# Optimization experiments

Measured on AMD Instinct MI355X. Metric: run time of the kernel, lower is better.

The kernel has to match this reference:

```python
import jax, jax.numpy as jnp
import numpy as np

B, TI, TO = 32, 128, 64
VI, VO = 32000, 32000
E, H, A = 256, 512, 512
EOS, BOS = 0, 1


def setup_inputs() -> dict:
    key = jax.random.key(0)
    ks = jax.random.split(key, 24)
    def p(k, shape):
        return jax.random.normal(k, shape, jnp.float32) * 0.05
    return {
        "inp": jax.random.randint(ks[0], (B, TI), 0, VI),
        "out": jax.random.randint(ks[1], (B, TO), 0, VO),
        "emb_inp": p(ks[2], (VI, E)),
        "emb_out": p(ks[3], (VO, E)),
        "enc_Wih_f": p(ks[4], (3 * H, E)),
        "enc_Whh_f": p(ks[5], (3 * H, H)),
        "enc_bih_f": p(ks[6], (3 * H,)),
        "enc_bhh_f": p(ks[7], (3 * H,)),
        "enc_Wih_b": p(ks[8], (3 * H, E)),
        "enc_Whh_b": p(ks[9], (3 * H, H)),
        "enc_bih_b": p(ks[10], (3 * H,)),
        "enc_bhh_b": p(ks[11], (3 * H,)),
        "dec_start_W": p(ks[12], (H, 2 * H)),
        "dec_start_b": p(ks[13], (H,)),
        "dec_Wih": p(ks[14], (3 * H, E + 2 * H)),
        "dec_Whh": p(ks[15], (3 * H, H)),
        "dec_bih": p(ks[16], (3 * H,)),
        "dec_bhh": p(ks[17], (3 * H,)),
        "attn_Wenc": p(ks[18], (A, 2 * H)),
        "attn_benc": p(ks[19], (A,)),
        "attn_Wdec": p(ks[20], (A, H)),
        "attn_bdec": p(ks[21], (A,)),
        "attn_v": p(ks[22], (A,)),
        "attn_vb": jnp.zeros((), jnp.float32),
        "logits_W": p(ks[23], (VO, 3 * H)),
        "logits_b": jnp.zeros((VO,), jnp.float32),
    }


def _gru_dir(x, Wih, bih, Whh, bhh, reverse):
    # x: [B,T,E]; precompute input projections once: [B,T,3H]
    xp = jnp.einsum('bte,ge->btg', x, Wih) + bih
    Hd = Whh.shape[1]
    def step(h, xt):
        gh = h @ Whh.T + bhh
        xr, xz, xn = jnp.split(xt, 3, -1)
        hr, hz, hn = jnp.split(gh, 3, -1)
        r = jax.nn.sigmoid(xr + hr)
        z = jax.nn.sigmoid(xz + hz)
        n = jnp.tanh(xn + r * hn)
        h_new = (1.0 - z) * n + z * h
        return h_new, h_new
    h0 = jnp.zeros((x.shape[0], Hd), x.dtype)
    _, hs = jax.lax.scan(step, h0, jnp.swapaxes(xp, 0, 1), reverse=reverse)
    return jnp.swapaxes(hs, 0, 1)  # [B,T,H]


def _forward(inp, out, emb_inp, emb_out,
             enc_Wih_f, enc_Whh_f, enc_bih_f, enc_bhh_f,
             enc_Wih_b, enc_Whh_b, enc_bih_b, enc_bhh_b,
             dec_start_W, dec_start_b, dec_Wih, dec_Whh, dec_bih, dec_bhh,
             attn_Wenc, attn_benc, attn_Wdec, attn_bdec, attn_v, attn_vb,
             logits_W, logits_b):
    x = emb_inp[inp]  # [B,TI,E]
    ef = _gru_dir(x, enc_Wih_f, enc_bih_f, enc_Whh_f, enc_bhh_f, False)
    eb = _gru_dir(x, enc_Wih_b, enc_bih_b, enc_Whh_b, enc_bhh_b, True)
    enc = jnp.concatenate([ef, eb], -1)  # [B,TI,2H]
    mask = (inp != EOS).astype(jnp.float32)
    lengths = jnp.minimum(mask.sum(1).astype(jnp.int32), TI - 1)
    last = enc[jnp.arange(enc.shape[0]), lengths]  # [B,2H]
    dec0 = last @ dec_start_W.T + dec_start_b  # [B,H]
    enc_proj = jnp.einsum('btd,ad->bta', enc, attn_Wenc) + attn_benc  # [B,TI,A]

    def attend(dec):
        dp = dec @ attn_Wdec.T + attn_bdec  # [B,A]
        s = jnp.tanh(enc_proj + dp[:, None, :]) @ attn_v + attn_vb  # [B,TI]
        s = jnp.where(mask > 0, s, -jnp.inf)
        pr = jax.nn.softmax(s, -1)
        return jnp.einsum('bt,btd->bd', pr, enc), pr

    a0, _ = attend(dec0)

    def step(carry, tok):
        h, a = carry
        e = emb_out[tok]  # [B,E]
        xg = jnp.concatenate([e, a], -1) @ dec_Wih.T + dec_bih
        hg = h @ dec_Whh.T + dec_bhh
        xr, xz, xn = jnp.split(xg, 3, -1)
        hr, hz, hn = jnp.split(hg, 3, -1)
        r = jax.nn.sigmoid(xr + hr)
        z = jax.nn.sigmoid(xz + hz)
        n = jnp.tanh(xn + r * hn)
        h_new = (1.0 - z) * n + z * h
        a_new, _ = attend(h_new)
        lg = jnp.concatenate([h_new, a_new], -1) @ logits_W.T + logits_b
        return (h_new, a_new), lg

    toks = jnp.swapaxes(out[:, :-1], 0, 1)  # [TO-1, B]
    _, lgs = jax.lax.scan(step, (dec0, a0), toks)  # [TO-1,B,VO]
    first = jnp.log(jax.nn.one_hot(jnp.full((out.shape[0],), BOS), VO) + 1e-9)
    return jnp.swapaxes(jnp.concatenate([first[None], lgs], 0), 0, 1)  # [B,TO,VO]


def reference(inp, out, emb_inp, emb_out,
              enc_Wih_f, enc_Whh_f, enc_bih_f, enc_bhh_f,
              enc_Wih_b, enc_Whh_b, enc_bih_b, enc_bhh_b,
              dec_start_W, dec_start_b, dec_Wih, dec_Whh, dec_bih, dec_bhh,
              attn_Wenc, attn_benc, attn_Wdec, attn_bdec, attn_v, attn_vb,
              logits_W, logits_b):
    return _forward(inp, out, emb_inp, emb_out,
                    enc_Wih_f, enc_Whh_f, enc_bih_f, enc_bhh_f,
                    enc_Wih_b, enc_Whh_b, enc_bih_b, enc_bhh_b,
                    dec_start_W, dec_start_b, dec_Wih, dec_Whh, dec_bih, dec_bhh,
                    attn_Wenc, attn_benc, attn_Wdec, attn_bdec, attn_v, attn_vb,
                    logits_W, logits_b)
```

## Files before the change

kernel.cpp:

```cpp
#include <hip/hip_runtime.h>
#include <math.h>
#include <stdint.h>

#define B_   32
#define TI_  128
#define TO_  64
#define E_   256
#define H_   512
#define A_   512
#define VO_  32000
#define G3_  1536
#define D2H_ 1024

using short8 = __attribute__((ext_vector_type(8))) short;
using f32x4  = __attribute__((ext_vector_type(4))) float;

__device__ __forceinline__ unsigned short f2bf(float x) {
  uint32_t u = __builtin_bit_cast(uint32_t, x);
  uint32_t r = (u + 0x7fffu + ((u >> 16) & 1u)) >> 16;
  return (unsigned short)r;
}


__global__ __launch_bounds__(256) void k_zero(float* __restrict__ p, int n) {
  int i = blockIdx.x * 256 + threadIdx.x;
  if (i < n) p[i] = 0.f;
}

__global__ __launch_bounds__(256) void k_zero_u16(unsigned short* __restrict__ p, int n) {
  int i = blockIdx.x * 256 + threadIdx.x;
  if (i < n) p[i] = 0;
}

__global__ __launch_bounds__(256) void k_cvt_bf16(const float* __restrict__ in,
                                                  unsigned short* __restrict__ out, int n8) {
  int i = blockIdx.x * 256 + threadIdx.x;
  if (i >= n8) return;
  float4 a = ((const float4*)in)[2 * i];
  float4 b = ((const float4*)in)[2 * i + 1];
  ushort4 lo = make_ushort4(f2bf(a.x), f2bf(a.y), f2bf(a.z), f2bf(a.w));
  ushort4 hi = make_ushort4(f2bf(b.x), f2bf(b.y), f2bf(b.z), f2bf(b.w));
  ((ushort4*)out)[2 * i] = lo;
  ((ushort4*)out)[2 * i + 1] = hi;
}

__global__ __launch_bounds__(256) void k_gather_x(const int* __restrict__ inp,
                                                  const float* __restrict__ emb,
                                                  float* __restrict__ x) {
  int idx = blockIdx.x * 256 + threadIdx.x;
  int total = B_ * TI_ * E_ / 4;
  if (idx >= total) return;
  int row = idx / (E_ / 4);
  int e4  = idx % (E_ / 4);
  int tok = inp[row];
  ((float4*)x)[idx] = ((const float4*)emb)[(size_t)tok * (E_ / 4) + e4];
}

__global__ __launch_bounds__(256) void k_gather_xe(const int* __restrict__ outidx,
                                                   const float* __restrict__ emb,
                                                   float* __restrict__ xe) {
  int idx = blockIdx.x * 256 + threadIdx.x;
  int total = 63 * B_ * E_ / 4;
  if (idx >= total) return;
  int row = idx / (E_ / 4);
  int e4  = idx % (E_ / 4);
  int i = row / B_, b = row % B_;
  int tok = outidx[b * TO_ + i];
  ((float4*)xe)[idx] = ((const float4*)emb)[(size_t)tok * (E_ / 4) + e4];
}

__global__ __launch_bounds__(256) void k_first(float* __restrict__ dout) {
  int idx = blockIdx.x * 256 + threadIdx.x;
  if (idx >= B_ * VO_) return;
  int b = idx / VO_, v = idx % VO_;
  dout[(size_t)b * TO_ * VO_ + v] = (v == 1) ? 0.f : -20.72326583694641f;
}


__global__ __launch_bounds__(256) void k_gemm128(
    const float* __restrict__ A, int lda,
    const float* __restrict__ W, int ldw,
    const float* __restrict__ bias,
    float* __restrict__ C, int M, int N, int K) {
  __shared__ float As[32][132];
  __shared__ float Bs[32][132];
  const int tid = threadIdx.x;
  const int m0 = blockIdx.y * 128, n0 = blockIdx.x * 128;
  const int tx = tid & 15, ty = tid >> 4;
  float acc[8][8];
#pragma unroll
  for (int i = 0; i < 8; ++i)
#pragma unroll
    for (int j = 0; j < 8; ++j) acc[i][j] = 0.f;

  for (int k0 = 0; k0 < K; k0 += 32) {
#pragma unroll
    for (int i = 0; i < 16; ++i) {
      int idx = tid + i * 256;
      int kk = idx & 31, mm = idx >> 5;
      int m = m0 + mm;
      As[kk][mm] = (m < M) ? A[(size_t)m * lda + k0 + kk] : 0.f;
      Bs[kk][mm] = W[(size_t)(n0 + mm) * ldw + k0 + kk];
    }
    __syncthreads();
#pragma unroll
    for (int kk = 0; kk < 32; ++kk) {
      float4 a0 = *(const float4*)&As[kk][ty * 8];
      float4 a1 = *(const float4*)&As[kk][ty * 8 + 4];
      float4 b0 = *(const float4*)&Bs[kk][tx * 8];
      float4 b1 = *(const float4*)&Bs[kk][tx * 8 + 4];
      float av[8] = {a0.x, a0.y, a0.z, a0.w, a1.x, a1.y, a1.z, a1.w};
      float bv[8] = {b0.x, b0.y, b0.z, b0.w, b1.x, b1.y, b1.z, b1.w};
#pragma unroll
      for (int i = 0; i < 8; ++i)
#pragma unroll
        for (int j = 0; j < 8; ++j) acc[i][j] = fmaf(av[i], bv[j], acc[i][j]);
    }
    __syncthreads();
  }

#pragma unroll
  for (int i = 0; i < 8; ++i) {
    int m = m0 + ty * 8 + i;
    if (m >= M) continue;
#pragma unroll
    for (int j = 0; j < 8; ++j) {
      int n = n0 + tx * 8 + j;
      C[(size_t)m * N + n] = acc[i][j] + bias[n];
    }
  }
}


__global__ __launch_bounds__(256) void k_logits_mfma(
    const unsigned short* __restrict__ A,
    const unsigned short* __restrict__ Bt,
    const float* __restrict__ bias,
    float* __restrict__ out) {
  __shared__ alignas(16) unsigned short As[128 * 32];
  __shared__ alignas(16) unsigned short Bs[128 * 32];
  const int tid = threadIdx.x;
  const int wave = tid >> 6, lane = tid & 63;
  const int m0 = blockIdx.y * 128, n0 = blockIdx.x * 128;
  const int wr = wave >> 1, wc = wave & 1;
  const int K = G3_;

  f32x4 acc[4][4];
#pragma unroll
  for (int i = 0; i < 4; ++i)
#pragma unroll
    for (int j = 0; j < 4; ++j) acc[i][j] = (f32x4){0.f, 0.f, 0.f, 0.f};

  const int srow = tid >> 2;
  const int sbyte = (tid & 3) * 16;
  const int fr = lane & 15;
  const int fkb = (lane >> 4) * 16;

  for (int k0 = 0; k0 < K; k0 += 32) {
#pragma unroll
    for (int rd = 0; rd < 2; ++rd) {
      int row = rd * 64 + srow;
      const char* ga = (const char*)(A + (size_t)(m0 + row) * K + k0) + sbyte;
      const char* gb = (const char*)(Bt + (size_t)(n0 + row) * K + k0) + sbyte;
      __builtin_amdgcn_global_load_lds(
          (const __attribute__((address_space(1))) uint32_t*)ga,
          (__attribute__((address_space(3))) uint32_t*)((char*)As + rd * 4096 + wave * 1024),
          16, 0, 0);
      __builtin_amdgcn_global_load_lds(
          (const __attribute__((address_space(1))) uint32_t*)gb,
          (__attribute__((address_space(3))) uint32_t*)((char*)Bs + rd * 4096 + wave * 1024),
          16, 0, 0);
    }
    __syncthreads();

    short8 af[4], bf[4];
#pragma unroll
    for (int i = 0; i < 4; ++i) {
      int ar = wr * 64 + i * 16 + fr;
      int bc = wc * 64 + i * 16 + fr;
      af[i] = *(const short8*)((const char*)As + ar * 64 + fkb);
      bf[i] = *(const short8*)((const char*)Bs + bc * 64 + fkb);
    }
#pragma unroll
    for (int i = 0; i < 4; ++i)
#pragma unroll
      for (int j = 0; j < 4; ++j)
        acc[i][j] = __builtin_amdgcn_mfma_f32_16x16x32_bf16(af[i], bf[j], acc[i][j], 0, 0, 0);
    __syncthreads();
  }

  const int crow = (lane >> 4) * 4, ccol = lane & 15;
#pragma unroll
  for (int i = 0; i < 4; ++i) {
#pragma unroll
    for (int r = 0; r < 4; ++r) {
      int m = m0 + wr * 64 + i * 16 + crow + r;
      if (m >= 63 * B_) continue;
      int b = m & 31, st = m >> 5;
      float* orow = out + ((size_t)b * TO_ + st + 1) * VO_;
#pragma unroll
      for (int j = 0; j < 4; ++j) {
        int n = n0 + wc * 64 + j * 16 + ccol;
        orow[n] = acc[i][j][r] + bias[n];
      }
    }
  }
}


__global__ __launch_bounds__(256) void k_enc_step(
    const float* __restrict__ hf_in, float* __restrict__ hf_out,
    const float* __restrict__ hb_in, float* __restrict__ hb_out,
    const float* __restrict__ xp_f, const float* __restrict__ xp_b,
    const float* __restrict__ Whh_f, const float* __restrict__ bhh_f,
    const float* __restrict__ Whh_b, const float* __restrict__ bhh_b,
    float* __restrict__ enc, int t) {
  __shared__ float hs[32 * 516];
  const int bid = blockIdx.x;
  const int dir = bid >> 6;
  const int slice = bid & 63;
  const float* h_in  = dir ? hb_in : hf_in;
  float*       h_out = dir ? hb_out : hf_out;
  const float* xp    = dir ? xp_b : xp_f;
  const float* Whh   = dir ? Whh_b : Whh_f;
  const float* bhh   = dir ? bhh_b : bhh_f;
  const int tt = dir ? (TI_ - 1 - t) : t;
  const int tid = threadIdx.x;

#pragma unroll
  for (int i = 0; i < 16; ++i) {
    int idx4 = tid + i * 256;
    int flat = idx4 * 4;
    int mm = flat >> 9, kk = flat & 511;
    *(float4*)&hs[mm * 516 + kk] = *(const float4*)(h_in + (size_t)mm * H_ + kk);
  }
  __syncthreads();

  const int m = tid & 31, c = tid >> 5;
  const int col = slice * 8 + c;
  const float* hrow = hs + m * 516;
  const float4* wr = (const float4*)(Whh + (size_t)col * H_);
  const float4* wz = (const float4*)(Whh + (size_t)(H_ + col) * H_);
  const float4* wn = (const float4*)(Whh + (size_t)(2 * H_ + col) * H_);
  float accr = 0.f, accz = 0.f, accn = 0.f;
#pragma unroll 4
  for (int k4 = 0; k4 < H_ / 4; ++k4) {
    float4 h4 = *(const float4*)(hrow + k4 * 4);
    float4 r = wr[k4], z = wz[k4], n = wn[k4];
    accr = fmaf(h4.x, r.x, fmaf(h4.y, r.y, fmaf(h4.z, r.z, fmaf(h4.w, r.w, accr))));
    accz = fmaf(h4.x, z.x, fmaf(h4.y, z.y, fmaf(h4.z, z.z, fmaf(h4.w, z.w, accz))));
    accn = fmaf(h4.x, n.x, fmaf(h4.y, n.y, fmaf(h4.z, n.z, fmaf(h4.w, n.w, accn))));
  }
  size_t xoff = ((size_t)m * TI_ + tt) * G3_ + col;
  float xr = xp[xoff], xz = xp[xoff + 512], xn = xp[xoff + 1024];
  float hr = accr + bhh[col];
  float hz = accz + bhh[512 + col];
  float hn = accn + bhh[1024 + col];
  float r = 1.f / (1.f + expf(-(xr + hr)));
  float z = 1.f / (1.f + expf(-(xz + hz)));
  float nn = tanhf(xn + r * hn);
  float hold = hrow[col];
  float hnew = (1.f - z) * nn + z * hold;
  h_out[m * H_ + col] = hnew;
  enc[((size_t)m * TI_ + tt) * D2H_ + dir * H_ + col] = hnew;
}


__global__ __launch_bounds__(256) void k_dec_step(
    const float* __restrict__ h_in, float* __restrict__ h_out,
    const float* __restrict__ a_in, const float* __restrict__ XE,
    const float* __restrict__ Wih, const float* __restrict__ Whh,
    const float* __restrict__ bhh,
    unsigned short* __restrict__ HA, int step) {
  __shared__ float buf[32 * 516];
  const int tid = threadIdx.x;
  const int m = tid & 31, c = tid >> 5;
  const int col = blockIdx.x * 8 + c;
  const float* hrow = buf + m * 516;
  float axr = 0.f, axz = 0.f, axn = 0.f, ahr = 0.f, ahz = 0.f, ahn = 0.f;

#pragma unroll
  for (int i = 0; i < 16; ++i) {
    int idx4 = tid + i * 256;
    int flat = idx4 * 4;
    int mm = flat >> 9, kk = flat & 511;
    *(float4*)&buf[mm * 516 + kk] = *(const float4*)(a_in + (size_t)mm * D2H_ + kk);
  }
  __syncthreads();
  {
    const float4* wr = (const float4*)(Wih + (size_t)col * 1280 + 256);
    const float4* wz = (const float4*)(Wih + (size_t)(512 + col) * 1280 + 256);
    const float4* wn = (const float4*)(Wih + (size_t)(1024 + col) * 1280 + 256);
#pragma unroll 4
    for (int k4 = 0; k4 < 128; ++k4) {
      float4 h4 = *(const float4*)(hrow + k4 * 4);
      float4 r = wr[k4], z = wz[k4], n = wn[k4];
      axr = fmaf(h4.x, r.x, fmaf(h4.y, r.y, fmaf(h4.z, r.z, fmaf(h4.w, r.w, axr))));
      axz = fmaf(h4.x, z.x, fmaf(h4.y, z.y, fmaf(h4.z, z.z, fmaf(h4.w, z.w, axz))));
      axn = fmaf(h4.x, n.x, fmaf(h4.y, n.y, fmaf(h4.z, n.z, fmaf(h4.w, n.w, axn))));
    }
  }
  __syncthreads();

#pragma unroll
  for (int i = 0; i < 16; ++i) {
    int idx4 = tid + i * 256;
    int flat = idx4 * 4;
    int mm = flat >> 9, kk = flat & 511;
    *(float4*)&buf[mm * 516 + kk] = *(const float4*)(a_in + (size_t)mm * D2H_ + 512 + kk);
  }
  __syncthreads();
  {
    const float4* wr = (const float4*)(Wih + (size_t)col * 1280 + 768);
    const float4* wz = (const float4*)(Wih + (size_t)(512 + col) * 1280 + 768);
    const float4* wn = (const float4*)(Wih + (size_t)(1024 + col) * 1280 + 768);
#pragma unroll 4
    for (int k4 = 0; k4 < 128; ++k4) {
      float4 h4 = *(const float4*)(hrow + k4 * 4);
      float4 r = wr[k4], z = wz[k4], n = wn[k4];
      axr = fmaf(h4.x, r.x, fmaf(h4.y, r.y, fmaf(h4.z, r.z, fmaf(h4.w, r.w, axr))));
      axz = fmaf(h4.x, z.x, fmaf(h4.y, z.y, fmaf(h4.z, z.z, fmaf(h4.w, z.w, axz))));
      axn = fmaf(h4.x, n.x, fmaf(h4.y, n.y, fmaf(h4.z, n.z, fmaf(h4.w, n.w, axn))));
    }
  }
  __syncthreads();

#pragma unroll
  for (int i = 0; i < 16; ++i) {
    int idx4 = tid + i * 256;
    int flat = idx4 * 4;
    int mm = flat >> 9, kk = flat & 511;
    *(float4*)&buf[mm * 516 + kk] = *(const float4*)(h_in + (size_t)mm * H_ + kk);
  }
  __syncthreads();
  {
    const float4* wr = (const float4*)(Whh + (size_t)col * H_);
    const float4* wz = (const float4*)(Whh + (size_t)(512 + col) * H_);
    const float4* wn = (const float4*)(Whh + (size_t)(1024 + col) * H_);
#pragma unroll 4
    for (int k4 = 0; k4 < 128; ++k4) {
      float4 h4 = *(const float4*)(hrow + k4 * 4);
      float4 r = wr[k4], z = wz[k4], n = wn[k4];
      ahr = fmaf(h4.x, r.x, fmaf(h4.y, r.y, fmaf(h4.z, r.z, fmaf(h4.w, r.w, ahr))));
      ahz = fmaf(h4.x, z.x, fmaf(h4.y, z.z, fmaf(h4.z, z.z, fmaf(h4.w, z.w, ahz))));
      ahn = fmaf(h4.x, n.x, fmaf(h4.y, n.y, fmaf(h4.z, n.z, fmaf(h4.w, n.w, ahn))));
    }
  }

  size_t xrow = ((size_t)step * B_ + m) * G3_;
  float xr = XE[xrow + col] + axr;
  float xz = XE[xrow + 512 + col] + axz;
  float xn = XE[xrow + 1024 + col] + axn;
  float hr = ahr + bhh[col];
  float hz = ahz + bhh[512 + col];
  float hn = ahn + bhh[1024 + col];
  float r = 1.f / (1.f + expf(-(xr + hr)));
  float z = 1.f / (1.f + expf(-(xz + hz)));
  float nn = tanhf(xn + r * hn);
  float hold = hrow[col];
  float hnew = (1.f - z) * nn + z * hold;
  h_out[m * H_ + col] = hnew;
  HA[xrow + col] = f2bf(hnew);
}


__global__ __launch_bounds__(256) void k_attend(
    const float* __restrict__ h_src, const float* __restrict__ enc,
    const float* __restrict__ enc_proj, const int* __restrict__ inp,
    const float* __restrict__ Wdec, const float* __restrict__ bdec,
    const float* __restrict__ v, const float* __restrict__ vb,
    float* __restrict__ a_out, unsigned short* __restrict__ HA, int step) {
  __shared__ float hq[512];
  __shared__ float dp[512];
  __shared__ float vv[512];
  __shared__ float part[256];
  __shared__ float sc[128];
  __shared__ float red[128];
  const int b = blockIdx.x, tid = threadIdx.x;

  hq[tid] = h_src[b * H_ + tid];
  hq[tid + 256] = h_src[b * H_ + 256 + tid];
  vv[tid] = v[tid];
  vv[tid + 256] = v[tid + 256];
  __syncthreads();

#pragma unroll
  for (int jj = 0; jj < 2; ++jj) {
    int j = tid + jj * 256;
    const float4* w4 = (const float4*)(Wdec + (size_t)j * H_);
    float acc = 0.f;
#pragma unroll 4
    for (int k4 = 0; k4 < H_ / 4; ++k4) {
      float4 w = w4[k4];
      float4 h4 = *(const float4*)&hq[k4 * 4];
      acc = fmaf(h4.x, w.x, fmaf(h4.y, w.y, fmaf(h4.z, w.z, fmaf(h4.w, w.w, acc))));
    }
    dp[j] = acc + bdec[j];
  }
  __syncthreads();

  {
    int t = tid & 127, half = tid >> 7;
    const float* ep = enc_proj + ((size_t)b * TI_ + t) * A_ + half * 256;
    const float* dph = dp + half * 256;
    const float* vh = vv + half * 256;
    float p = 0.f;
    for (int a = 0; a < 256; ++a) p = fmaf(vh[a], tanhf(ep[a] + dph[a]), p);
    part[tid] = p;
  }
  __syncthreads();
  if (tid < 128) {
    float s = part[tid] + part[tid + 128] + vb[0];
    if (inp[b * TI_ + tid] == 0) s = -INFINITY;
    sc[tid] = s;
    red[tid] = s;
  }
  __syncthreads();
  for (int o = 64; o > 0; o >>= 1) {
    if (tid < o) red[tid] = fmaxf(red[tid], red[tid + o]);
    __syncthreads();
  }
  float mx = red[0];
  __syncthreads();
  if (tid < 128) {
    float e = expf(sc[tid] - mx);
    sc[tid] = e;
    red[tid] = e;
  }
  __syncthreads();
  for (int o = 64; o > 0; o >>= 1) {
    if (tid < o) red[tid] += red[tid + o];
    __syncthreads();
  }
  float inv = 1.f / red[0];
  __syncthreads();

  float4 acc = make_float4(0.f, 0.f, 0.f, 0.f);
  const float4* e4p = (const float4*)(enc + (size_t)b * TI_ * D2H_) + tid;
#pragma unroll 4
  for (int t2 = 0; t2 < TI_; ++t2) {
    float pr = sc[t2] * inv;
    float4 ev = e4p[(size_t)t2 * (D2H_ / 4)];
    acc.x = fmaf(pr, ev.x, acc.x);
    acc.y = fmaf(pr, ev.y, acc.y);
    acc.z = fmaf(pr, ev.z, acc.z);
    acc.w = fmaf(pr, ev.w, acc.w);
  }
  *(float4*)(a_out + (size_t)b * D2H_ + tid * 4) = acc;
  if (step >= 0) {
    unsigned short* hp = HA + ((size_t)step * B_ + b) * G3_ + H_ + tid * 4;
    *(ushort4*)hp = make_ushort4(f2bf(acc.x), f2bf(acc.y), f2bf(acc.z), f2bf(acc.w));
  }
}


__global__ __launch_bounds__(256) void k_dec0(
    const int* __restrict__ inp, const float* __restrict__ enc,
    const float* __restrict__ Wst, const float* __restrict__ bst,
    float* __restrict__ h0) {
  __shared__ float last[1024];
  __shared__ int redi[128];
  __shared__ int slen;
  const int b = blockIdx.x, tid = threadIdx.x;
  if (tid < 128) redi[tid] = (inp[b * TI_ + tid] != 0) ? 1 : 0;
  __syncthreads();
  for (int o = 64; o > 0; o >>= 1) {
    if (tid < o) redi[tid] += redi[tid + o];
    __syncthreads();
  }
  if (tid == 0) slen = min(redi[0], TI_ - 1);
  __syncthreads();
  int len = slen;
#pragma unroll
  for (int i = 0; i < 4; ++i)
    last[tid + i * 256] = enc[((size_t)b * TI_ + len) * D2H_ + tid + i * 256];
  __syncthreads();
#pragma unroll
  for (int jj = 0; jj < 2; ++jj) {
    int j = tid + jj * 256;
    const float4* w4 = (const float4*)(Wst + (size_t)j * D2H_);
    float acc = 0.f;
#pragma unroll 4
    for (int k4 = 0; k4 < D2H_ / 4; ++k4) {
      float4 w = w4[k4];
      float4 l4 = *(const float4*)&last[k4 * 4];
      acc = fmaf(l4.x, w.x, fmaf(l4.y, w.y, fmaf(l4.z, w.z, fmaf(l4.w, w.w, acc))));
    }
    h0[b * H_ + j] = acc + bst[j];
  }
}


extern "C" void kernel_launch(void* const* d_in, const int* in_sizes, int n_in,
                              void* d_out, int out_size, void* d_ws, size_t ws_size,
                              hipStream_t stream) {
  const int*   inp     = (const int*)d_in[0];
  const int*   outi    = (const int*)d_in[1];
  const float* emb_inp = (const float*)d_in[2];
  const float* emb_out = (const float*)d_in[3];
  const float* eWih_f  = (const float*)d_in[4];
  const float* eWhh_f  = (const float*)d_in[5];
  const float* ebih_f  = (const float*)d_in[6];
  const float* ebhh_f  = (const float*)d_in[7];
  const float* eWih_b  = (const float*)d_in[8];
  const float* eWhh_b  = (const float*)d_in[9];
  const float* ebih_b  = (const float*)d_in[10];
  const float* ebhh_b  = (const float*)d_in[11];
  const float* dsW     = (const float*)d_in[12];
  const float* dsb     = (const float*)d_in[13];
  const float* dWih    = (const float*)d_in[14];
  const float* dWhh    = (const float*)d_in[15];
  const float* dbih    = (const float*)d_in[16];
  const float* dbhh    = (const float*)d_in[17];
  const float* aWenc   = (const float*)d_in[18];
  const float* abenc   = (const float*)d_in[19];
  const float* aWdec   = (const float*)d_in[20];
  const float* abdec   = (const float*)d_in[21];
  const float* av      = (const float*)d_in[22];
  const float* avb     = (const float*)d_in[23];
  const float* lW      = (const float*)d_in[24];
  const float* lb      = (const float*)d_in[25];
  float* dout = (float*)d_out;

  float* ws = (float*)d_ws;
  size_t off = 0;
  auto alloc = [&](size_t n) { float* p = ws + off; off += n; return p; };
  float* x    = alloc((size_t)B_ * TI_ * E_);
  float* xp_f = alloc((size_t)B_ * TI_ * G3_);
  float* xp_b = alloc((size_t)B_ * TI_ * G3_);
  float* enc  = alloc((size_t)B_ * TI_ * D2H_);
  float* encp = alloc((size_t)B_ * TI_ * A_);
  float* xe   = alloc((size_t)63 * B_ * E_);
  float* XE   = alloc((size_t)63 * B_ * G3_);
  unsigned short* HAb = (unsigned short*)alloc((size_t)2048 * G3_ / 2);
  unsigned short* lWb = (unsigned short*)alloc((size_t)VO_ * G3_ / 2);
  float* hf0  = alloc(B_ * H_);
  float* hf1  = alloc(B_ * H_);
  float* hb0  = alloc(B_ * H_);
  float* hb1  = alloc(B_ * H_);
  float* hd0  = alloc(B_ * H_);
  float* hd1  = alloc(B_ * H_);
  float* adec = alloc(B_ * D2H_);

  k_zero<<<(2 * B_ * H_ + 255) / 256, 256, 0, stream>>>(hf0, B_ * H_);
  k_zero<<<(2 * B_ * H_ + 255) / 256, 256, 0, stream>>>(hb0, B_ * H_);
  k_zero_u16<<<(32 * G3_) / 256, 256, 0, stream>>>(HAb + (size_t)2016 * G3_, 32 * G3_);

  k_cvt_bf16<<<((VO_ * G3_ / 8) + 255) / 256, 256, 0, stream>>>(lW, lWb, VO_ * G3_ / 8);

  k_gather_x<<<(B_ * TI_ * E_ / 4 + 255) / 256, 256, 0, stream>>>(inp, emb_inp, x);
  dim3 g1(G3_ / 128, (B_ * TI_) / 128);
  k_gemm128<<<g1, 256, 0, stream>>>(x, E_, eWih_f, E_, ebih_f, xp_f, B_ * TI_, G3_, E_);
  k_gemm128<<<g1, 256, 0, stream>>>(x, E_, eWih_b, E_, ebih_b, xp_b, B_ * TI_, G3_, E_);

  float* hfb[2] = {hf0, hf1};
  float* hbb[2] = {hb0, hb1};
  for (int t = 0; t < TI_; ++t) {
    k_enc_step<<<128, 256, 0, stream>>>(hfb[t & 1], hfb[(t + 1) & 1],
                                        hbb[t & 1], hbb[(t + 1) & 1],
                                        xp_f, xp_b, eWhh_f, ebhh_f, eWhh_b, ebhh_b,
                                        enc, t);
  }

  dim3 g2(A_ / 128, (B_ * TI_) / 128);
  k_gemm128<<<g2, 256, 0, stream>>>(enc, D2H_, aWenc, D2H_, abenc, encp, B_ * TI_, A_, D2H_);

  k_dec0<<<B_, 256, 0, stream>>>(inp, enc, dsW, dsb, hd0);
  k_attend<<<B_, 256, 0, stream>>>(hd0, enc, encp, inp, aWdec, abdec, av, avb, adec, HAb, -1);

  k_gather_xe<<<(63 * B_ * E_ / 4 + 255) / 256, 256, 0, stream>>>(outi, emb_out, xe);
  dim3 g3(G3_ / 128, (63 * B_ + 127) / 128);
  k_gemm128<<<g3, 256, 0, stream>>>(xe, E_, dWih, E_ + D2H_, dbih, XE, 63 * B_, G3_, E_);

  float* hdb[2] = {hd0, hd1};
  for (int i = 0; i < 63; ++i) {
    k_dec_step<<<64, 256, 0, stream>>>(hdb[i & 1], hdb[(i + 1) & 1], adec, XE,
                                       dWih, dWhh, dbhh, HAb, i);
    k_attend<<<B_, 256, 0, stream>>>(hdb[(i + 1) & 1], enc, encp, inp,
                                     aWdec, abdec, av, avb, adec, HAb, i);
  }

  dim3 g4(VO_ / 128, 16);
  k_logits_mfma<<<g4, 256, 0, stream>>>(HAb, lWb, lb, dout);

  k_first<<<(B_ * VO_ + 255) / 256, 256, 0, stream>>>(dout);
}
```

Measured before the change: 10.89 ms.

## Persistent encoder/decoder kernels, bf16 MFMA GEMMs, precomputed attention-context projections

Replaces the per-timestep encoder and decoder launches with two persistent kernels, one block per (direction, batch) or per batch row, that keep the hidden state in LDS and loop over time internally. All dense GEMMs move from the fp32 SIMT tiled kernel to a templated bf16 MFMA kernel, with weights and activations converted to bf16 up front. Folds the attention-context part of the decoder input projection into a precomputed per-encoder-position table (encWT), so each step does a 128-length dot product instead of a 1024-wide matvec. This removes hundreds of kernel launches and fp32 FMA throughput limits, at the cost of bf16 rounding in the recurrent state, approximate sigmoid/tanh, and only 32 to 64 blocks active during the recurrence.

```diff
diff --git a/kernel.cpp b/kernel.cpp
--- a/kernel.cpp
+++ b/kernel.cpp
@@ -14,22 +14,40 @@
 
 using short8 = __attribute__((ext_vector_type(8))) short;
 using f32x4  = __attribute__((ext_vector_type(4))) float;
+typedef __attribute__((ext_vector_type(2))) __bf16 bf16x2_t;
 
 __device__ __forceinline__ unsigned short f2bf(float x) {
   uint32_t u = __builtin_bit_cast(uint32_t, x);
   uint32_t r = (u + 0x7fffu + ((u >> 16) & 1u)) >> 16;
   return (unsigned short)r;
 }
-
-
-__global__ __launch_bounds__(256) void k_zero(float* __restrict__ p, int n) {
+__device__ __forceinline__ uint32_t pack2(float lo, float hi) {
+  return (uint32_t)f2bf(lo) | ((uint32_t)f2bf(hi) << 16);
+}
+__device__ __forceinline__ float bflo(uint32_t u) { return __builtin_bit_cast(float, u << 16); }
+__device__ __forceinline__ float bfhi(uint32_t u) { return __builtin_bit_cast(float, u & 0xffff0000u); }
+
+#if __has_builtin(__builtin_amdgcn_fdot2_f32_bf16)
+__device__ __forceinline__ float dot2bf(uint32_t a, uint32_t b, float c) {
+  return __builtin_amdgcn_fdot2_f32_bf16(__builtin_bit_cast(bf16x2_t, a),
+                                         __builtin_bit_cast(bf16x2_t, b), c, false);
+}
+#else
+__device__ __forceinline__ float dot2bf(uint32_t a, uint32_t b, float c) {
+  return fmaf(bfhi(a), bfhi(b), fmaf(bflo(a), bflo(b), c));
+}
+#endif
+
+__device__ __forceinline__ float sigf(float x) {
+  return __builtin_amdgcn_rcpf(1.f + __expf(-x));
+}
+__device__ __forceinline__ float tanhf_(float x) {
+  return fmaf(-2.f, __builtin_amdgcn_rcpf(1.f + __expf(2.f * x)), 1.f);
+}
+
+__global__ __launch_bounds__(256) void k_init(unsigned short* __restrict__ tail) {
   int i = blockIdx.x * 256 + threadIdx.x;
-  if (i < n) p[i] = 0.f;
-}
-
-__global__ __launch_bounds__(256) void k_zero_u16(unsigned short* __restrict__ p, int n) {
-  int i = blockIdx.x * 256 + threadIdx.x;
-  if (i < n) p[i] = 0;
+  if (i < 32 * G3_) tail[i] = 0;
 }
 
 __global__ __launch_bounds__(256) void k_cvt_bf16(const float* __restrict__ in,
@@ -38,35 +56,61 @@
   if (i >= n8) return;
   float4 a = ((const float4*)in)[2 * i];
   float4 b = ((const float4*)in)[2 * i + 1];
-  ushort4 lo = make_ushort4(f2bf(a.x), f2bf(a.y), f2bf(a.z), f2bf(a.w));
-  ushort4 hi = make_ushort4(f2bf(b.x), f2bf(b.y), f2bf(b.z), f2bf(b.w));
-  ((ushort4*)out)[2 * i] = lo;
-  ((ushort4*)out)[2 * i + 1] = hi;
-}
-
-__global__ __launch_bounds__(256) void k_gather_x(const int* __restrict__ inp,
-                                                  const float* __restrict__ emb,
-                                                  float* __restrict__ x) {
+  uint4 o = { pack2(a.x, a.y), pack2(a.z, a.w), pack2(b.x, b.y), pack2(b.z, b.w) };
+  ((uint4*)out)[i] = o;
+}
+
+__global__ __launch_bounds__(256) void k_cvt_multi(
+    const float* __restrict__ i0, unsigned short* __restrict__ o0,
+    const float* __restrict__ i1, unsigned short* __restrict__ o1,
+    const float* __restrict__ i2, unsigned short* __restrict__ o2,
+    const float* __restrict__ i3, unsigned short* __restrict__ o3,
+    const float* __restrict__ i4, unsigned short* __restrict__ o4,
+    const float* __restrict__ i5, unsigned short* __restrict__ o5,
+    const float* __restrict__ i6, unsigned short* __restrict__ o6,
+    const float* __restrict__ i7, unsigned short* __restrict__ o7) {
+  int u = blockIdx.x * 256 + threadIdx.x;
+  const float* in; unsigned short* out; int lu;
+  if      (u < 98304)  { in = i0; out = o0; lu = u; }
+  else if (u < 196608) { in = i1; out = o1; lu = u - 98304; }
+  else if (u < 294912) { in = i2; out = o2; lu = u - 196608; }
+  else if (u < 327680) { in = i3; out = o3; lu = u - 294912; }
+  else if (u < 573440) { in = i4; out = o4; lu = u - 327680; }
+  else if (u < 638976) { in = i5; out = o5; lu = u - 573440; }
+  else if (u < 688128) { in = i6; out = o6; lu = u - 638976; }
+  else if (u < 737280) { in = i7; out = o7; lu = u - 688128; }
+  else return;
+  float4 a = ((const float4*)in)[2 * lu];
+  float4 b = ((const float4*)in)[2 * lu + 1];
+  uint4 o = { pack2(a.x, a.y), pack2(a.z, a.w), pack2(b.x, b.y), pack2(b.z, b.w) };
+  ((uint4*)out)[lu] = o;
+}
+
+__global__ __launch_bounds__(256) void k_gather_xb(const int* __restrict__ inp,
+                                                   const float* __restrict__ emb,
+                                                   unsigned short* __restrict__ xb) {
   int idx = blockIdx.x * 256 + threadIdx.x;
-  int total = B_ * TI_ * E_ / 4;
-  if (idx >= total) return;
-  int row = idx / (E_ / 4);
-  int e4  = idx % (E_ / 4);
+  if (idx >= 4096 * 32) return;
+  int row = idx >> 5, e8 = idx & 31;
   int tok = inp[row];
-  ((float4*)x)[idx] = ((const float4*)emb)[(size_t)tok * (E_ / 4) + e4];
-}
-
-__global__ __launch_bounds__(256) void k_gather_xe(const int* __restrict__ outidx,
-                                                   const float* __restrict__ emb,
-                                                   float* __restrict__ xe) {
+  const float4* s = (const float4*)(emb + (size_t)tok * E_ + e8 * 8);
+  float4 a = s[0], b = s[1];
+  uint4 o = { pack2(a.x, a.y), pack2(a.z, a.w), pack2(b.x, b.y), pack2(b.z, b.w) };
+  ((uint4*)xb)[idx] = o;
+}
+
+__global__ __launch_bounds__(256) void k_gather_xeb(const int* __restrict__ outi,
+                                                    const float* __restrict__ emb,
+                                                    unsigned short* __restrict__ xeb) {
   int idx = blockIdx.x * 256 + threadIdx.x;
-  int total = 63 * B_ * E_ / 4;
-  if (idx >= total) return;
-  int row = idx / (E_ / 4);
-  int e4  = idx % (E_ / 4);
-  int i = row / B_, b = row % B_;
-  int tok = outidx[b * TO_ + i];
-  ((float4*)xe)[idx] = ((const float4*)emb)[(size_t)tok * (E_ / 4) + e4];
+  if (idx >= 2016 * 32) return;
+  int row = idx >> 5, e8 = idx & 31;
+  int i = row >> 5, b = row & 31;
+  int tok = outi[b * TO_ + i];
+  const float4* s = (const float4*)(emb + (size_t)tok * E_ + e8 * 8);
+  float4 a = s[0], bb = s[1];
+  uint4 o = { pack2(a.x, a.y), pack2(a.z, a.w), pack2(bb.x, bb.y), pack2(bb.z, bb.w) };
+  ((uint4*)xeb)[idx] = o;
 }
 
 __global__ __launch_bounds__(256) void k_first(float* __restrict__ dout) {
@@ -76,74 +120,18 @@
   dout[(size_t)b * TO_ * VO_ + v] = (v == 1) ? 0.f : -20.72326583694641f;
 }
 
-
-__global__ __launch_bounds__(256) void k_gemm128(
-    const float* __restrict__ A, int lda,
-    const float* __restrict__ W, int ldw,
+template <int MODE>
+__global__ __launch_bounds__(256) void k_bgemm(
+    const unsigned short* __restrict__ A, int lda,
+    const unsigned short* __restrict__ Bt, int ldb,
     const float* __restrict__ bias,
-    float* __restrict__ C, int M, int N, int K) {
-  __shared__ float As[32][132];
-  __shared__ float Bs[32][132];
-  const int tid = threadIdx.x;
-  const int m0 = blockIdx.y * 128, n0 = blockIdx.x * 128;
-  const int tx = tid & 15, ty = tid >> 4;
-  float acc[8][8];
-#pragma unroll
-  for (int i = 0; i < 8; ++i)
-#pragma unroll
-    for (int j = 0; j < 8; ++j) acc[i][j] = 0.f;
-
-  for (int k0 = 0; k0 < K; k0 += 32) {
-#pragma unroll
-    for (int i = 0; i < 16; ++i) {
-      int idx = tid + i * 256;
-      int kk = idx & 31, mm = idx >> 5;
-      int m = m0 + mm;
-      As[kk][mm] = (m < M) ? A[(size_t)m * lda + k0 + kk] : 0.f;
-      Bs[kk][mm] = W[(size_t)(n0 + mm) * ldw + k0 + kk];
-    }
-    __syncthreads();
-#pragma unroll
-    for (int kk = 0; kk < 32; ++kk) {
-      float4 a0 = *(const float4*)&As[kk][ty * 8];
-      float4 a1 = *(const float4*)&As[kk][ty * 8 + 4];
-      float4 b0 = *(const float4*)&Bs[kk][tx * 8];
-      float4 b1 = *(const float4*)&Bs[kk][tx * 8 + 4];
-      float av[8] = {a0.x, a0.y, a0.z, a0.w, a1.x, a1.y, a1.z, a1.w};
-      float bv[8] = {b0.x, b0.y, b0.z, b0.w, b1.x, b1.y, b1.z, b1.w};
-#pragma unroll
-      for (int i = 0; i < 8; ++i)
-#pragma unroll
-        for (int j = 0; j < 8; ++j) acc[i][j] = fmaf(av[i], bv[j], acc[i][j]);
-    }
-    __syncthreads();
-  }
-
-#pragma unroll
-  for (int i = 0; i < 8; ++i) {
-    int m = m0 + ty * 8 + i;
-    if (m >= M) continue;
-#pragma unroll
-    for (int j = 0; j < 8; ++j) {
-      int n = n0 + tx * 8 + j;
-      C[(size_t)m * N + n] = acc[i][j] + bias[n];
-    }
-  }
-}
-
-
-__global__ __launch_bounds__(256) void k_logits_mfma(
-    const unsigned short* __restrict__ A,
-    const unsigned short* __restrict__ Bt,
-    const float* __restrict__ bias,
-    float* __restrict__ out) {
+    void* __restrict__ Cv, int ldc, int M, int N, int K) {
   __shared__ alignas(16) unsigned short As[128 * 32];
   __shared__ alignas(16) unsigned short Bs[128 * 32];
   const int tid = threadIdx.x;
   const int wave = tid >> 6, lane = tid & 63;
   const int m0 = blockIdx.y * 128, n0 = blockIdx.x * 128;
   const int wr = wave >> 1, wc = wave & 1;
-  const int K = G3_;
 
   f32x4 acc[4][4];
 #pragma unroll
@@ -160,8 +148,9 @@
 #pragma unroll
     for (int rd = 0; rd < 2; ++rd) {
       int row = rd * 64 + srow;
-      const char* ga = (const char*)(A + (size_t)(m0 + row) * K + k0) + sbyte;
-      const char* gb = (const char*)(Bt + (size_t)(n0 + row) * K + k0) + sbyte;
+      int ra = min(m0 + row, M - 1);
+      const char* ga = (const char*)(A + (size_t)ra * lda + k0) + sbyte;
+      const char* gb = (const char*)(Bt + (size_t)(n0 + row) * ldb + k0) + sbyte;
       __builtin_amdgcn_global_load_lds(
           (const __attribute__((address_space(1))) uint32_t*)ga,
           (__attribute__((address_space(3))) uint32_t*)((char*)As + rd * 4096 + wave * 1024),
@@ -195,298 +184,293 @@
 #pragma unroll
     for (int r = 0; r < 4; ++r) {
       int m = m0 + wr * 64 + i * 16 + crow + r;
-      if (m >= 63 * B_) continue;
-      int b = m & 31, st = m >> 5;
-      float* orow = out + ((size_t)b * TO_ + st + 1) * VO_;
+      if (m >= M) continue;
 #pragma unroll
       for (int j = 0; j < 4; ++j) {
         int n = n0 + wc * 64 + j * 16 + ccol;
-        orow[n] = acc[i][j][r] + bias[n];
+        float v = acc[i][j][r] + (bias ? bias[n] : 0.f);
+        if (MODE == 0) {
+          ((float*)Cv)[(size_t)m * ldc + n] = v;
+        } else if (MODE == 1) {
+          ((unsigned short*)Cv)[(size_t)m * ldc + n] = f2bf(v);
+        } else {
+          int bb = m & 31, st = m >> 5;
+          ((float*)Cv)[((size_t)bb * TO_ + st + 1) * VO_ + n] = v;
+        }
       }
     }
   }
 }
 
-
-__global__ __launch_bounds__(256) void k_enc_step(
-    const float* __restrict__ hf_in, float* __restrict__ hf_out,
-    const float* __restrict__ hb_in, float* __restrict__ hb_out,
-    const float* __restrict__ xp_f, const float* __restrict__ xp_b,
-    const float* __restrict__ Whh_f, const float* __restrict__ bhh_f,
-    const float* __restrict__ Whh_b, const float* __restrict__ bhh_b,
-    float* __restrict__ enc, int t) {
-  __shared__ float hs[32 * 516];
+__global__ __launch_bounds__(256) void k_encoder(
+    const unsigned short* __restrict__ xpb_f, const unsigned short* __restrict__ xpb_b,
+    const unsigned short* __restrict__ Whhb_f, const float* __restrict__ bhh_f,
+    const unsigned short* __restrict__ Whhb_b, const float* __restrict__ bhh_b,
+    unsigned short* __restrict__ encb) {
+  __shared__ alignas(16) float h[512];
+  __shared__ uint32_t hb2[256];
+  __shared__ uint32_t xrow[768];
   const int bid = blockIdx.x;
-  const int dir = bid >> 6;
-  const int slice = bid & 63;
-  const float* h_in  = dir ? hb_in : hf_in;
-  float*       h_out = dir ? hb_out : hf_out;
-  const float* xp    = dir ? xp_b : xp_f;
-  const float* Whh   = dir ? Whh_b : Whh_f;
-  const float* bhh   = dir ? bhh_b : bhh_f;
-  const int tt = dir ? (TI_ - 1 - t) : t;
+  const int dir = bid >> 5, b = bid & 31;
+  const unsigned short* xpb = dir ? xpb_b : xpb_f;
+  const unsigned short* Whh = dir ? Whhb_b : Whhb_f;
+  const float* bhh = dir ? bhh_b : bhh_f;
   const int tid = threadIdx.x;
-
-#pragma unroll
-  for (int i = 0; i < 16; ++i) {
-    int idx4 = tid + i * 256;
-    int flat = idx4 * 4;
-    int mm = flat >> 9, kk = flat & 511;
-    *(float4*)&hs[mm * 516 + kk] = *(const float4*)(h_in + (size_t)mm * H_ + kk);
-  }
+  const int c0 = 2 * tid, c1 = c0 + 1;
+
+  h[c0] = 0.f; h[c1] = 0.f; hb2[tid] = 0u;
+  const float br0 = bhh[c0], br1 = bhh[c1];
+  const float bz0 = bhh[512 + c0], bz1 = bhh[512 + c1];
+  const float bn0 = bhh[1024 + c0], bn1 = bhh[1024 + c1];
+  const uint4* w_r0 = (const uint4*)(Whh + (size_t)c0 * 512);
+  const uint4* w_r1 = (const uint4*)(Whh + (size_t)c1 * 512);
+  const uint4* w_z0 = (const uint4*)(Whh + (size_t)(512 + c0) * 512);
+  const uint4* w_z1 = (const uint4*)(Whh + (size_t)(512 + c1) * 512);
+  const uint4* w_n0 = (const uint4*)(Whh + (size_t)(1024 + c0) * 512);
+  const uint4* w_n1 = (const uint4*)(Whh + (size_t)(1024 + c1) * 512);
+
+  for (int t = 0; t < TI_; ++t) {
+    const int tt = dir ? (TI_ - 1 - t) : t;
+    const uint32_t* xr = (const uint32_t*)(xpb + (size_t)(b * 128 + tt) * G3_);
+    xrow[tid] = xr[tid];
+    xrow[tid + 256] = xr[tid + 256];
+    xrow[tid + 512] = xr[tid + 512];
+    __syncthreads();
+
+    float ar0 = 0.f, ar1 = 0.f, az0 = 0.f, az1 = 0.f, an0 = 0.f, an1 = 0.f;
+#pragma unroll 4
+    for (int k = 0; k < 64; ++k) {
+      uint32_t p0 = hb2[4 * k], p1 = hb2[4 * k + 1], p2 = hb2[4 * k + 2], p3 = hb2[4 * k + 3];
+      uint4 u;
+      u = w_r0[k]; ar0 = dot2bf(p0, u.x, ar0); ar0 = dot2bf(p1, u.y, ar0);
+                   ar0 = dot2bf(p2, u.z, ar0); ar0 = dot2bf(p3, u.w, ar0);
+      u = w_r1[k]; ar1 = dot2bf(p0, u.x, ar1); ar1 = dot2bf(p1, u.y, ar1);
+                   ar1 = dot2bf(p2, u.z, ar1); ar1 = dot2bf(p3, u.w, ar1);
+      u = w_z0[k]; az0 = dot2bf(p0, u.x, az0); az0 = dot2bf(p1, u.y, az0);
+                   az0 = dot2bf(p2, u.z, az0); az0 = dot2bf(p3, u.w, az0);
+      u = w_z1[k]; az1 = dot2bf(p0, u.x, az1); az1 = dot2bf(p1, u.y, az1);
+                   az1 = dot2bf(p2, u.z, az1); az1 = dot2bf(p3, u.w, az1);
+      u = w_n0[k]; an0 = dot2bf(p0, u.x, an0); an0 = dot2bf(p1, u.y, an0);
+                   an0 = dot2bf(p2, u.z, an0); an0 = dot2bf(p3, u.w, an0);
+      u = w_n1[k]; an1 = dot2bf(p0, u.x, an1); an1 = dot2bf(p1, u.y, an1);
+                   an1 = dot2bf(p2, u.z, an1); an1 = dot2bf(p3, u.w, an1);
+    }
+    uint32_t uxr = xrow[tid], uxz = xrow[256 + tid], uxn = xrow[512 + tid];
+    float r0 = sigf(bflo(uxr) + ar0 + br0);
+    float r1 = sigf(bfhi(uxr) + ar1 + br1);
+    float z0 = sigf(bflo(uxz) + az0 + bz0);
+    float z1 = sigf(bfhi(uxz) + az1 + bz1);
+    float n0 = tanhf_(bflo(uxn) + r0 * (an0 + bn0));
+    float n1 = tanhf_(bfhi(uxn) + r1 * (an1 + bn1));
+    float hn0 = (1.f - z0) * n0 + z0 * h[c0];
+    float hn1 = (1.f - z1) * n1 + z1 * h[c1];
+    ((uint32_t*)encb)[(size_t)(b * 128 + tt) * 512 + dir * 256 + tid] = pack2(hn0, hn1);
+    __syncthreads();
+    h[c0] = hn0; h[c1] = hn1; hb2[tid] = pack2(hn0, hn1);
+    __syncthreads();
+  }
+}
+
+__global__ __launch_bounds__(256) void k_decoder(
+    const int* __restrict__ inp,
+    const unsigned short* __restrict__ encb,
+    const unsigned short* __restrict__ encpb,
+    const float* __restrict__ XE,
+    const unsigned short* __restrict__ encWT,
+    const float* __restrict__ dsW, const float* __restrict__ dsb,
+    const unsigned short* __restrict__ dWhhb, const float* __restrict__ dbhh,
+    const unsigned short* __restrict__ aWdecb, const float* __restrict__ abdec,
+    const float* __restrict__ abenc,
+    const float* __restrict__ av, const float* __restrict__ avb,
+    unsigned short* __restrict__ HAb) {
+  __shared__ alignas(16) uint32_t encp_s[128 * 257];
+  __shared__ alignas(16) float h[512];
+  __shared__ uint32_t hb2[256];
+  __shared__ float pr[128];
+  __shared__ uint32_t prb2[64];
+  __shared__ float dp[512];
+  __shared__ float red[256];
+  __shared__ float msk[128];
+  __shared__ alignas(16) float vstage[1024];
+  const int b = blockIdx.x, tid = threadIdx.x;
+  const int c0 = 2 * tid, c1 = c0 + 1;
+
+  {
+    const uint32_t* epg = (const uint32_t*)(encpb + (size_t)b * 128 * 512);
+#pragma unroll 4
+    for (int i = 0; i < 128; ++i) {
+      int u = tid + i * 256;
+      encp_s[(u >> 8) * 257 + (u & 255)] = epg[u];
+    }
+  }
+  if (tid < 128) msk[tid] = (inp[b * TI_ + tid] != 0) ? 1.f : 0.f;
   __syncthreads();
-
-  const int m = tid & 31, c = tid >> 5;
-  const int col = slice * 8 + c;
-  const float* hrow = hs + m * 516;
-  const float4* wr = (const float4*)(Whh + (size_t)col * H_);
-  const float4* wz = (const float4*)(Whh + (size_t)(H_ + col) * H_);
-  const float4* wn = (const float4*)(Whh + (size_t)(2 * H_ + col) * H_);
-  float accr = 0.f, accz = 0.f, accn = 0.f;
+  if (tid < 64) {
+    float s = msk[tid] + msk[tid + 64];
+#pragma unroll
+    for (int off = 32; off > 0; off >>= 1) s += __shfl_xor(s, off);
+    if (tid == 0) red[0] = s;
+  }
+  __syncthreads();
+  const int len = min((int)red[0], TI_ - 1);
+
+  {
+    const uint32_t* lrow = (const uint32_t*)(encb + (size_t)(b * 128 + len) * D2H_);
+    uint32_t u0 = lrow[tid], u1 = lrow[256 + tid];
+    vstage[c0] = bflo(u0); vstage[c1] = bfhi(u0);
+    vstage[512 + c0] = bflo(u1); vstage[512 + c1] = bfhi(u1);
+    __syncthreads();
+    const float4* w0 = (const float4*)(dsW + (size_t)c0 * D2H_);
+    const float4* w1 = (const float4*)(dsW + (size_t)c1 * D2H_);
+    float a0 = 0.f, a1 = 0.f;
 #pragma unroll 4
-  for (int k4 = 0; k4 < H_ / 4; ++k4) {
-    float4 h4 = *(const float4*)(hrow + k4 * 4);
-    float4 r = wr[k4], z = wz[k4], n = wn[k4];
-    accr = fmaf(h4.x, r.x, fmaf(h4.y, r.y, fmaf(h4.z, r.z, fmaf(h4.w, r.w, accr))));
-    accz = fmaf(h4.x, z.x, fmaf(h4.y, z.y, fmaf(h4.z, z.z, fmaf(h4.w, z.w, accz))));
-    accn = fmaf(h4.x, n.x, fmaf(h4.y, n.y, fmaf(h4.z, n.z, fmaf(h4.w, n.w, accn))));
-  }
-  size_t xoff = ((size_t)m * TI_ + tt) * G3_ + col;
-  float xr = xp[xoff], xz = xp[xoff + 512], xn = xp[xoff + 1024];
-  float hr = accr + bhh[col];
-  float hz = accz + bhh[512 + col];
-  float hn = accn + bhh[1024 + col];
-  float r = 1.f / (1.f + expf(-(xr + hr)));
-  float z = 1.f / (1.f + expf(-(xz + hz)));
-  float nn = tanhf(xn + r * hn);
-  float hold = hrow[col];
-  float hnew = (1.f - z) * nn + z * hold;
-  h_out[m * H_ + col] = hnew;
-  enc[((size_t)m * TI_ + tt) * D2H_ + dir * H_ + col] = hnew;
-}
-
-
-__global__ __launch_bounds__(256) void k_dec_step(
-    const float* __restrict__ h_in, float* __restrict__ h_out,
-    const float* __restrict__ a_in, const float* __restrict__ XE,
-    const float* __restrict__ Wih, const float* __restrict__ Whh,
-    const float* __restrict__ bhh,
-    unsigned short* __restrict__ HA, int step) {
-  __shared__ float buf[32 * 516];
-  const int tid = threadIdx.x;
-  const int m = tid & 31, c = tid >> 5;
-  const int col = blockIdx.x * 8 + c;
-  const float* hrow = buf + m * 516;
-  float axr = 0.f, axz = 0.f, axn = 0.f, ahr = 0.f, ahz = 0.f, ahn = 0.f;
-
-#pragma unroll
-  for (int i = 0; i < 16; ++i) {
-    int idx4 = tid + i * 256;
-    int flat = idx4 * 4;
-    int mm = flat >> 9, kk = flat & 511;
-    *(float4*)&buf[mm * 516 + kk] = *(const float4*)(a_in + (size_t)mm * D2H_ + kk);
-  }
-  __syncthreads();
-  {
-    const float4* wr = (const float4*)(Wih + (size_t)col * 1280 + 256);
-    const float4* wz = (const float4*)(Wih + (size_t)(512 + col) * 1280 + 256);
-    const float4* wn = (const float4*)(Wih + (size_t)(1024 + col) * 1280 + 256);
+    for (int k = 0; k < 256; ++k) {
+      float4 l = *(const float4*)&vstage[4 * k];
+      float4 q0 = w0[k], q1 = w1[k];
+      a0 = fmaf(l.x, q0.x, fmaf(l.y, q0.y, fmaf(l.z, q0.z, fmaf(l.w, q0.w, a0))));
+      a1 = fmaf(l.x, q1.x, fmaf(l.y, q1.y, fmaf(l.z, q1.z, fmaf(l.w, q1.w, a1))));
+    }
+    float h0v = a0 + dsb[c0], h1v = a1 + dsb[c1];
+    __syncthreads();
+    h[c0] = h0v; h[c1] = h1v; hb2[tid] = pack2(h0v, h1v);
+    vstage[tid] = av[tid];
+    vstage[256 + tid] = av[256 + tid];
+    __syncthreads();
+  }
+
+  auto attend = [&](int step) {
+    {
+      const uint4* w0 = (const uint4*)(aWdecb + (size_t)c0 * 512);
+      const uint4* w1 = (const uint4*)(aWdecb + (size_t)c1 * 512);
+      float d0 = 0.f, d1 = 0.f;
+#pragma unroll 8
+      for (int k = 0; k < 64; ++k) {
+        uint32_t p0 = hb2[4 * k], p1 = hb2[4 * k + 1], p2 = hb2[4 * k + 2], p3 = hb2[4 * k + 3];
+        uint4 u0 = w0[k];
+        d0 = dot2bf(p0, u0.x, d0); d0 = dot2bf(p1, u0.y, d0);
+        d0 = dot2bf(p2, u0.z, d0); d0 = dot2bf(p3, u0.w, d0);
+        uint4 u1 = w1[k];
+        d1 = dot2bf(p0, u1.x, d1); d1 = dot2bf(p1, u1.y, d1);
+        d1 = dot2bf(p2, u1.z, d1); d1 = dot2bf(p3, u1.w, d1);
+      }
+      dp[c0] = d0 + abdec[c0] + abenc[c0];
+      dp[c1] = d1 + abdec[c1] + abenc[c1];
+    }
+    __syncthreads();
+    {
+      int t = tid & 127, half = tid >> 7;
+      const uint32_t* ep = encp_s + t * 257 + half * 128;
+      const float* dph = dp + half * 256;
+      const float* vh = vstage + half * 256;
+      float s = 0.f;
 #pragma unroll 4
-    for (int k4 = 0; k4 < 128; ++k4) {
-      float4 h4 = *(const float4*)(hrow + k4 * 4);
-      float4 r = wr[k4], z = wz[k4], n = wn[k4];
-      axr = fmaf(h4.x, r.x, fmaf(h4.y, r.y, fmaf(h4.z, r.z, fmaf(h4.w, r.w, axr))));
-      axz = fmaf(h4.x, z.x, fmaf(h4.y, z.y, fmaf(h4.z, z.z, fmaf(h4.w, z.w, axz))));
-      axn = fmaf(h4.x, n.x, fmaf(h4.y, n.y, fmaf(h4.z, n.z, fmaf(h4.w, n.w, axn))));
-    }
-  }
-  __syncthreads();
-
-#pragma unroll
-  for (int i = 0; i < 16; ++i) {
-    int idx4 = tid + i * 256;
-    int flat = idx4 * 4;
-    int mm = flat >> 9, kk = flat & 511;
-    *(float4*)&buf[mm * 516 + kk] = *(const float4*)(a_in + (size_t)mm * D2H_ + 512 + kk);
-  }
-  __syncthreads();
-  {
-    const float4* wr = (const float4*)(Wih + (size_t)col * 1280 + 768);
-    const float4* wz = (const float4*)(Wih + (size_t)(512 + col) * 1280 + 768);
-    const float4* wn = (const float4*)(Wih + (size_t)(1024 + col) * 1280 + 768);
+      for (int a2 = 0; a2 < 128; ++a2) {
+        uint32_t u = ep[a2];
+        s = fmaf(vh[2 * a2],     tanhf_(bflo(u) + dph[2 * a2]),     s);
+        s = fmaf(vh[2 * a2 + 1], tanhf_(bfhi(u) + dph[2 * a2 + 1]), s);
+      }
+      red[tid] = s;
+    }
+    __syncthreads();
+    if (tid < 128) {
+      float s = red[tid] + red[tid + 128] + avb[0];
+      red[tid] = (msk[tid] > 0.f) ? s : -1e30f;
+    }
+    __syncthreads();
+    if (tid < 64) {
+      float m = fmaxf(red[tid], red[tid + 64]);
+#pragma unroll
+      for (int off = 32; off > 0; off >>= 1) m = fmaxf(m, __shfl_xor(m, off));
+      if (tid == 0) dp[0] = m;
+    }
+    __syncthreads();
+    float mx = dp[0];
+    if (tid < 128) red[tid] = __expf(red[tid] - mx);
+    __syncthreads();
+    if (tid < 64) {
+      float s2 = red[tid] + red[tid + 64];
+#pragma unroll
+      for (int off = 32; off > 0; off >>= 1) s2 += __shfl_xor(s2, off);
+      if (tid == 0) dp[1] = s2;
+    }
+    __syncthreads();
+    float inv = __builtin_amdgcn_rcpf(dp[1]);
+    if (tid < 128) pr[tid] = red[tid] * inv;
+    __syncthreads();
+    if (tid < 64) prb2[tid] = pack2(pr[2 * tid], pr[2 * tid + 1]);
+    if (step >= 0) {
+      const uint32_t* eb = (const uint32_t*)(encb + (size_t)b * 128 * D2H_);
+      float x0 = 0.f, x1 = 0.f, x2 = 0.f, x3 = 0.f;
 #pragma unroll 4
-    for (int k4 = 0; k4 < 128; ++k4) {
-      float4 h4 = *(const float4*)(hrow + k4 * 4);
-      float4 r = wr[k4], z = wz[k4], n = wn[k4];
-      axr = fmaf(h4.x, r.x, fmaf(h4.y, r.y, fmaf(h4.z, r.z, fmaf(h4.w, r.w, axr))));
-      axz = fmaf(h4.x, z.x, fmaf(h4.y, z.y, fmaf(h4.z, z.z, fmaf(h4.w, z.w, axz))));
-      axn = fmaf(h4.x, n.x, fmaf(h4.y, n.y, fmaf(h4.z, n.z, fmaf(h4.w, n.w, axn))));
-    }
-  }
-  __syncthreads();
-
-#pragma unroll
-  for (int i = 0; i < 16; ++i) {
-    int idx4 = tid + i * 256;
-    int flat = idx4 * 4;
-    int mm = flat >> 9, kk = flat & 511;
-    *(float4*)&buf[mm * 516 + kk] = *(const float4*)(h_in + (size_t)mm * H_ + kk);
-  }
-  __syncthreads();
-  {
-    const float4* wr = (const float4*)(Whh + (size_t)col * H_);
-    const float4* wz = (const float4*)(Whh + (size_t)(512 + col) * H_);
-    const float4* wn = (const float4*)(Whh + (size_t)(1024 + col) * H_);
-#pragma unroll 4
-    for (int k4 = 0; k4 < 128; ++k4) {
-      float4 h4 = *(const float4*)(hrow + k4 * 4);
-      float4 r = wr[k4], z = wz[k4], n = wn[k4];
-      ahr = fmaf(h4.x, r.x, fmaf(h4.y, r.y, fmaf(h4.z, r.z, fmaf(h4.w, r.w, ahr))));
-      ahz = fmaf(h4.x, z.x, fmaf(h4.y, z.z, fmaf(h4.z, z.z, fmaf(h4.w, z.w, ahz))));
-      ahn = fmaf(h4.x, n.x, fmaf(h4.y, n.y, fmaf(h4.z, n.z, fmaf(h4.w, n.w, ahn))));
-    }
-  }
-
-  size_t xrow = ((size_t)step * B_ + m) * G3_;
-  float xr = XE[xrow + col] + axr;
-  float xz = XE[xrow + 512 + col] + axz;
-  float xn = XE[xrow + 1024 + col] + axn;
-  float hr = ahr + bhh[col];
-  float hz = ahz + bhh[512 + col];
-  float hn = ahn + bhh[1024 + col];
-  float r = 1.f / (1.f + expf(-(xr + hr)));
-  float z = 1.f / (1.f + expf(-(xz + hz)));
-  float nn = tanhf(xn + r * hn);
-  float hold = hrow[col];
-  float hnew = (1.f - z) * nn + z * hold;
-  h_out[m * H_ + col] = hnew;
-  HA[xrow + col] = f2bf(hnew);
-}
-
-
-__global__ __launch_bounds__(256) void k_attend(
-    const float* __restrict__ h_src, const float* __restrict__ enc,
-    const float* __restrict__ enc_proj, const int* __restrict__ inp,
-    const float* __restrict__ Wdec, const float* __restrict__ bdec,
-    const float* __restrict__ v, const float* __restrict__ vb,
-    float* __restrict__ a_out, unsigned short* __restrict__ HA, int step) {
-  __shared__ float hq[512];
-  __shared__ float dp[512];
-  __shared__ float vv[512];
-  __shared__ float part[256];
-  __shared__ float sc[128];
-  __shared__ float red[128];
-  const int b = blockIdx.x, tid = threadIdx.x;
-
-  hq[tid] = h_src[b * H_ + tid];
-  hq[tid + 256] = h_src[b * H_ + 256 + tid];
-  vv[tid] = v[tid];
-  vv[tid + 256] = v[tid + 256];
-  __syncthreads();
-
-#pragma unroll
-  for (int jj = 0; jj < 2; ++jj) {
-    int j = tid + jj * 256;
-    const float4* w4 = (const float4*)(Wdec + (size_t)j * H_);
-    float acc = 0.f;
-#pragma unroll 4
-    for (int k4 = 0; k4 < H_ / 4; ++k4) {
-      float4 w = w4[k4];
-      float4 h4 = *(const float4*)&hq[k4 * 4];
-      acc = fmaf(h4.x, w.x, fmaf(h4.y, w.y, fmaf(h4.z, w.z, fmaf(h4.w, w.w, acc))));
-    }
-    dp[j] = acc + bdec[j];
-  }
-  __syncthreads();
-
-  {
-    int t = tid & 127, half = tid >> 7;
-    const float* ep = enc_proj + ((size_t)b * TI_ + t) * A_ + half * 256;
-    const float* dph = dp + half * 256;
-    const float* vh = vv + half * 256;
-    float p = 0.f;
-    for (int a = 0; a < 256; ++a) p = fmaf(vh[a], tanhf(ep[a] + dph[a]), p);
-    part[tid] = p;
-  }
-  __syncthreads();
-  if (tid < 128) {
-    float s = part[tid] + part[tid + 128] + vb[0];
-    if (inp[b * TI_ + tid] == 0) s = -INFINITY;
-    sc[tid] = s;
-    red[tid] = s;
-  }
-  __syncthreads();
-  for (int o = 64; o > 0; o >>= 1) {
-    if (tid < o) red[tid] = fmaxf(red[tid], red[tid + o]);
-    __syncthreads();
-  }
-  float mx = red[0];
-  __syncthreads();
-  if (tid < 128) {
-    float e = expf(sc[tid] - mx);
-    sc[tid] = e;
-    red[tid] = e;
-  }
-  __syncthreads();
-  for (int o = 64; o > 0; o >>= 1) {
-    if (tid < o) red[tid] += red[tid + o];
-    __syncthreads();
-  }
-  float inv = 1.f / red[0];
-  __syncthreads();
-
-  float4 acc = make_float4(0.f, 0.f, 0.f, 0.f);
-  const float4* e4p = (const float4*)(enc + (size_t)b * TI_ * D2H_) + tid;
-#pragma unroll 4
-  for (int t2 = 0; t2 < TI_; ++t2) {
-    float pr = sc[t2] * inv;
-    float4 ev = e4p[(size_t)t2 * (D2H_ / 4)];
-    acc.x = fmaf(pr, ev.x, acc.x);
-    acc.y = fmaf(pr, ev.y, acc.y);
-    acc.z = fmaf(pr, ev.z, acc.z);
-    acc.w = fmaf(pr, ev.w, acc.w);
-  }
-  *(float4*)(a_out + (size_t)b * D2H_ + tid * 4) = acc;
-  if (step >= 0) {
-    unsigned short* hp = HA + ((size_t)step * B_ + b) * G3_ + H_ + tid * 4;
-    *(ushort4*)hp = make_ushort4(f2bf(acc.x), f2bf(acc.y), f2bf(acc.z), f2bf(acc.w));
-  }
-}
-
-
-__global__ __launch_bounds__(256) void k_dec0(
-    const int* __restrict__ inp, const float* __restrict__ enc,
-    const float* __restrict__ Wst, const float* __restrict__ bst,
-    float* __restrict__ h0) {
-  __shared__ float last[1024];
-  __shared__ int redi[128];
-  __shared__ int slen;
-  const int b = blockIdx.x, tid = threadIdx.x;
-  if (tid < 128) redi[tid] = (inp[b * TI_ + tid] != 0) ? 1 : 0;
-  __syncthreads();
-  for (int o = 64; o > 0; o >>= 1) {
-    if (tid < o) redi[tid] += redi[tid + o];
-    __syncthreads();
-  }
-  if (tid == 0) slen = min(redi[0], TI_ - 1);
-  __syncthreads();
-  int len = slen;
-#pragma unroll
-  for (int i = 0; i < 4; ++i)
-    last[tid + i * 256] = enc[((size_t)b * TI_ + len) * D2H_ + tid + i * 256];
-  __syncthreads();
-#pragma unroll
-  for (int jj = 0; jj < 2; ++jj) {
-    int j = tid + jj * 256;
-    const float4* w4 = (const float4*)(Wst + (size_t)j * D2H_);
-    float acc = 0.f;
-#pragma unroll 4
-    for (int k4 = 0; k4 < D2H_ / 4; ++k4) {
-      float4 w = w4[k4];
-      float4 l4 = *(const float4*)&last[k4 * 4];
-      acc = fmaf(l4.x, w.x, fmaf(l4.y, w.y, fmaf(l4.z, w.z, fmaf(l4.w, w.w, acc))));
-    }
-    h0[b * H_ + j] = acc + bst[j];
+      for (int t = 0; t < 128; ++t) {
+        float p = pr[t];
+        uint32_t u0 = eb[(size_t)t * 512 + tid];
+        uint32_t u1 = eb[(size_t)t * 512 + 256 + tid];
+        x0 = fmaf(p, bflo(u0), x0); x1 = fmaf(p, bfhi(u0), x1);
+        x2 = fmaf(p, bflo(u1), x2); x3 = fmaf(p, bfhi(u1), x3);
+      }
+      uint32_t* hrow = (uint32_t*)(HAb + ((size_t)step * 32 + b) * G3_);
+      hrow[256 + tid] = pack2(x0, x1);
+      hrow[512 + tid] = pack2(x2, x3);
+    }
+    __syncthreads();
+  };
+
+  auto gru = [&](int i) {
+    float xa[6], ha[6];
+#pragma unroll
+    for (int g = 0; g < 3; ++g) {
+      const uint4* e0 = (const uint4*)(encWT + (size_t)(g * 512 + c0) * 4096 + b * 128);
+      const uint4* e1 = (const uint4*)(encWT + (size_t)(g * 512 + c1) * 4096 + b * 128);
+      float s0 = 0.f, s1 = 0.f;
+#pragma unroll
+      for (int k = 0; k < 16; ++k) {
+        uint32_t p0 = prb2[4 * k], p1 = prb2[4 * k + 1], p2 = prb2[4 * k + 2], p3 = prb2[4 * k + 3];
+        uint4 u0 = e0[k];
+        s0 = dot2bf(p0, u0.x, s0); s0 = dot2bf(p1, u0.y, s0);
+        s0 = dot2bf(p2, u0.z, s0); s0 = dot2bf(p3, u0.w, s0);
+        uint4 u1 = e1[k];
+        s1 = dot2bf(p0, u1.x, s1); s1 = dot2bf(p1, u1.y, s1);
+        s1 = dot2bf(p2, u1.z, s1); s1 = dot2bf(p3, u1.w, s1);
+      }
+      xa[g * 2] = s0; xa[g * 2 + 1] = s1;
+    }
+#pragma unroll
+    for (int g = 0; g < 3; ++g) {
+      const uint4* w0 = (const uint4*)(dWhhb + (size_t)(g * 512 + c0) * 512);
+      const uint4* w1 = (const uint4*)(dWhhb + (size_t)(g * 512 + c1) * 512);
+      float s0 = 0.f, s1 = 0.f;
+#pragma unroll 8
+      for (int k = 0; k < 64; ++k) {
+        uint32_t p0 = hb2[4 * k], p1 = hb2[4 * k + 1], p2 = hb2[4 * k + 2], p3 = hb2[4 * k + 3];
+        uint4 u0 = w0[k];
+        s0 = dot2bf(p0, u0.x, s0); s0 = dot2bf(p1, u0.y, s0);
+        s0 = dot2bf(p2, u0.z, s0); s0 = dot2bf(p3, u0.w, s0);
+        uint4 u1 = w1[k];
+        s1 = dot2bf(p0, u1.x, s1); s1 = dot2bf(p1, u1.y, s1);
+        s1 = dot2bf(p2, u1.z, s1); s1 = dot2bf(p3, u1.w, s1);
+      }
+      ha[g * 2] = s0; ha[g * 2 + 1] = s1;
+    }
+    const float* xrow = XE + ((size_t)i * 32 + b) * G3_;
+    float r0 = sigf(xrow[c0] + xa[0] + ha[0] + dbhh[c0]);
+    float r1 = sigf(xrow[c1] + xa[1] + ha[1] + dbhh[c1]);
+    float z0 = sigf(xrow[512 + c0] + xa[2] + ha[2] + dbhh[512 + c0]);
+    float z1 = sigf(xrow[512 + c1] + xa[3] + ha[3] + dbhh[512 + c1]);
+    float n0 = tanhf_(xrow[1024 + c0] + xa[4] + r0 * (ha[4] + dbhh[1024 + c0]));
+    float n1 = tanhf_(xrow[1024 + c1] + xa[5] + r1 * (ha[5] + dbhh[1024 + c1]));
+    float hn0 = (1.f - z0) * n0 + z0 * h[c0];
+    float hn1 = (1.f - z1) * n1 + z1 * h[c1];
+    ((uint32_t*)(HAb + ((size_t)i * 32 + b) * G3_))[tid] = pack2(hn0, hn1);
+    __syncthreads();
+    h[c0] = hn0; h[c1] = hn1; hb2[tid] = pack2(hn0, hn1);
+    __syncthreads();
+  };
+
+  attend(-1);
+  for (int i = 0; i < 63; ++i) {
+    gru(i);
+    attend(i);
   }
 }
 
@@ -522,66 +506,69 @@
   const float* lb      = (const float*)d_in[25];
   float* dout = (float*)d_out;
 
-  float* ws = (float*)d_ws;
+  char* ws = (char*)d_ws;
   size_t off = 0;
-  auto alloc = [&](size_t n) { float* p = ws + off; off += n; return p; };
-  float* x    = alloc((size_t)B_ * TI_ * E_);
-  float* xp_f = alloc((size_t)B_ * TI_ * G3_);
-  float* xp_b = alloc((size_t)B_ * TI_ * G3_);
-  float* enc  = alloc((size_t)B_ * TI_ * D2H_);
-  float* encp = alloc((size_t)B_ * TI_ * A_);
-  float* xe   = alloc((size_t)63 * B_ * E_);
-  float* XE   = alloc((size_t)63 * B_ * G3_);
-  unsigned short* HAb = (unsigned short*)alloc((size_t)2048 * G3_ / 2);
-  unsigned short* lWb = (unsigned short*)alloc((size_t)VO_ * G3_ / 2);
-  float* hf0  = alloc(B_ * H_);
-  float* hf1  = alloc(B_ * H_);
-  float* hb0  = alloc(B_ * H_);
-  float* hb1  = alloc(B_ * H_);
-  float* hd0  = alloc(B_ * H_);
-  float* hd1  = alloc(B_ * H_);
-  float* adec = alloc(B_ * D2H_);
-
-  k_zero<<<(2 * B_ * H_ + 255) / 256, 256, 0, stream>>>(hf0, B_ * H_);
-  k_zero<<<(2 * B_ * H_ + 255) / 256, 256, 0, stream>>>(hb0, B_ * H_);
-  k_zero_u16<<<(32 * G3_) / 256, 256, 0, stream>>>(HAb + (size_t)2016 * G3_, 32 * G3_);
-
-  k_cvt_bf16<<<((VO_ * G3_ / 8) + 255) / 256, 256, 0, stream>>>(lW, lWb, VO_ * G3_ / 8);
-
-  k_gather_x<<<(B_ * TI_ * E_ / 4 + 255) / 256, 256, 0, stream>>>(inp, emb_inp, x);
-  dim3 g1(G3_ / 128, (B_ * TI_) / 128);
-  k_gemm128<<<g1, 256, 0, stream>>>(x, E_, eWih_f, E_, ebih_f, xp_f, B_ * TI_, G3_, E_);
-  k_gemm128<<<g1, 256, 0, stream>>>(x, E_, eWih_b, E_, ebih_b, xp_b, B_ * TI_, G3_, E_);
-
-  float* hfb[2] = {hf0, hf1};
-  float* hbb[2] = {hb0, hb1};
-  for (int t = 0; t < TI_; ++t) {
-    k_enc_step<<<128, 256, 0, stream>>>(hfb[t & 1], hfb[(t + 1) & 1],
-                                        hbb[t & 1], hbb[(t + 1) & 1],
-                                        xp_f, xp_b, eWhh_f, ebhh_f, eWhh_b, ebhh_b,
-                                        enc, t);
-  }
-
-  dim3 g2(A_ / 128, (B_ * TI_) / 128);
-  k_gemm128<<<g2, 256, 0, stream>>>(enc, D2H_, aWenc, D2H_, abenc, encp, B_ * TI_, A_, D2H_);
-
-  k_dec0<<<B_, 256, 0, stream>>>(inp, enc, dsW, dsb, hd0);
-  k_attend<<<B_, 256, 0, stream>>>(hd0, enc, encp, inp, aWdec, abdec, av, avb, adec, HAb, -1);
-
-  k_gather_xe<<<(63 * B_ * E_ / 4 + 255) / 256, 256, 0, stream>>>(outi, emb_out, xe);
-  dim3 g3(G3_ / 128, (63 * B_ + 127) / 128);
-  k_gemm128<<<g3, 256, 0, stream>>>(xe, E_, dWih, E_ + D2H_, dbih, XE, 63 * B_, G3_, E_);
-
-  float* hdb[2] = {hd0, hd1};
-  for (int i = 0; i < 63; ++i) {
-    k_dec_step<<<64, 256, 0, stream>>>(hdb[i & 1], hdb[(i + 1) & 1], adec, XE,
-                                       dWih, dWhh, dbhh, HAb, i);
-    k_attend<<<B_, 256, 0, stream>>>(hdb[(i + 1) & 1], enc, encp, inp,
-                                     aWdec, abdec, av, avb, adec, HAb, i);
-  }
-
-  dim3 g4(VO_ / 128, 16);
-  k_logits_mfma<<<g4, 256, 0, stream>>>(HAb, lWb, lb, dout);
-
-  k_first<<<(B_ * VO_ + 255) / 256, 256, 0, stream>>>(dout);
-}
+  auto alloc = [&](size_t bytes) {
+    void* p = ws + off;
+    off += (bytes + 255) & ~(size_t)255;
+    return p;
+  };
+  unsigned short* xb      = (unsigned short*)alloc((size_t)4096 * 256 * 2);
+  unsigned short* xeb     = (unsigned short*)alloc((size_t)2016 * 256 * 2);
+  unsigned short* xpb_f   = (unsigned short*)alloc((size_t)4096 * G3_ * 2);
+  unsigned short* xpb_b   = (unsigned short*)alloc((size_t)4096 * G3_ * 2);
+  unsigned short* encb    = (unsigned short*)alloc((size_t)4096 * D2H_ * 2);
+  unsigned short* encpb   = (unsigned short*)alloc((size_t)4096 * 512 * 2);
+  unsigned short* encWT   = (unsigned short*)alloc((size_t)G3_ * 4096 * 2);
+  float*          XE      = (float*)alloc((size_t)2016 * G3_ * 4);
+  unsigned short* HAb     = (unsigned short*)alloc((size_t)2048 * G3_ * 2);
+  unsigned short* lWb     = (unsigned short*)alloc((size_t)VO_ * G3_ * 2);
+  unsigned short* eWhhb_f = (unsigned short*)alloc((size_t)G3_ * 512 * 2);
+  unsigned short* eWhhb_b = (unsigned short*)alloc((size_t)G3_ * 512 * 2);
+  unsigned short* dWhhb   = (unsigned short*)alloc((size_t)G3_ * 512 * 2);
+  unsigned short* aWdecb  = (unsigned short*)alloc((size_t)512 * 512 * 2);
+  unsigned short* dWihb   = (unsigned short*)alloc((size_t)G3_ * 1280 * 2);
+  unsigned short* aWencb  = (unsigned short*)alloc((size_t)512 * D2H_ * 2);
+  unsigned short* eWihb_f = (unsigned short*)alloc((size_t)G3_ * 256 * 2);
+  unsigned short* eWihb_b = (unsigned short*)alloc((size_t)G3_ * 256 * 2);
+
+  k_init<<<192, 256, 0, stream>>>(HAb + (size_t)2016 * G3_);
+  k_cvt_multi<<<2880, 256, 0, stream>>>(eWhh_f, eWhhb_f, eWhh_b, eWhhb_b,
+                                        dWhh, dWhhb, aWdec, aWdecb,
+                                        dWih, dWihb, aWenc, aWencb,
+                                        eWih_f, eWihb_f, eWih_b, eWihb_b);
+  k_cvt_bf16<<<24000, 256, 0, stream>>>(lW, lWb, VO_ * G3_ / 8);
+
+  k_gather_xb<<<512, 256, 0, stream>>>(inp, emb_inp, xb);
+  k_gather_xeb<<<252, 256, 0, stream>>>(outi, emb_out, xeb);
+
+  {
+    dim3 g(12, 32);
+    k_bgemm<1><<<g, 256, 0, stream>>>(xb, 256, eWihb_f, 256, ebih_f, xpb_f, G3_, 4096, G3_, 256);
+    k_bgemm<1><<<g, 256, 0, stream>>>(xb, 256, eWihb_b, 256, ebih_b, xpb_b, G3_, 4096, G3_, 256);
+  }
+
+  k_encoder<<<64, 256, 0, stream>>>(xpb_f, xpb_b, eWhhb_f, ebhh_f, eWhhb_b, ebhh_b, encb);
+
+  {
+    dim3 g(4, 32);
+    k_bgemm<1><<<g, 256, 0, stream>>>(encb, D2H_, aWencb, D2H_, nullptr, encpb, 512, 4096, 512, D2H_);
+  }
+  {
+    dim3 g(32, 12);
+    k_bgemm<1><<<g, 256, 0, stream>>>(dWihb + 256, 1280, encb, D2H_, nullptr, encWT, 4096, G3_, 4096, D2H_);
+  }
+  {
+    dim3 g(12, 16);
+    k_bgemm<0><<<g, 256, 0, stream>>>(xeb, 256, dWihb, 1280, dbih, XE, G3_, 2016, G3_, 256);
+  }
+
+  k_decoder<<<32, 256, 0, stream>>>(inp, encb, encpb, XE, encWT, dsW, dsb,
+                                    dWhhb, dbhh, aWdecb, abdec, abenc, av, avb, HAb);
+
+  {
+    dim3 g(250, 16);
+    k_bgemm<3><<<g, 256, 0, stream>>>(HAb, G3_, lWb, G3_, lb, dout, 0, 2016, VO_, G3_);
+  }
+  k_first<<<4000, 256, 0, stream>>>(dout);
+}
```

Result: slower. 12.00 ms (+10.2%).
